# Performance work log

Hardware: AMD Instinct MI355X
Metric: run time of the kernel (lower is better)

Reference implementation:

```python
import jax, jax.numpy as jnp
import numpy as np

B, T, D = 2048, 240, 90  # batch, seq_len (hard-coded 240 in module), hidden
NCLS = 40


def setup_inputs() -> dict:
    key = jax.random.key(0)
    ks = jax.random.split(key, 7)
    s = 1.0 / np.sqrt(D)          # torch LSTMCell init bound
    so = 1.0 / np.sqrt(T * D)     # torch Linear init bound
    x = jax.random.normal(ks[0], (B, T, D), dtype=jnp.float32)
    W_ih = jax.random.uniform(ks[1], (4 * D, D), minval=-s, maxval=s, dtype=jnp.float32)
    W_hh = jax.random.uniform(ks[2], (4 * D, D), minval=-s, maxval=s, dtype=jnp.float32)
    b_ih = jax.random.uniform(ks[3], (4 * D,), minval=-s, maxval=s, dtype=jnp.float32)
    b_hh = jax.random.uniform(ks[4], (4 * D,), minval=-s, maxval=s, dtype=jnp.float32)
    W_out = jax.random.uniform(ks[5], (NCLS, T * D), minval=-so, maxval=so, dtype=jnp.float32)
    b_out = jax.random.uniform(ks[6], (NCLS,), minval=-so, maxval=so, dtype=jnp.float32)
    return {"x": x, "W_ih": W_ih, "W_hh": W_hh, "b_ih": b_ih, "b_hh": b_hh,
            "W_out": W_out, "b_out": b_out}


def reference(x, W_ih, W_hh, b_ih, b_hh, W_out, b_out):
    # The torch loop calls LSTMCell(x[:, i]) with DEFAULT zero (h0, c0) every
    # step -> no recurrence. W_hh @ h0 == 0 and f * c0 == 0, so:
    #   gates = x_t @ W_ih^T + b_ih + b_hh ; gate order i, f, g, o
    gates = jnp.einsum('btd,gd->btg', x, W_ih) + b_ih + b_hh  # [B, T, 4D]
    i_g, _f_g, g_g, o_g = jnp.split(gates, 4, axis=-1)
    c = jax.nn.sigmoid(i_g) * jnp.tanh(g_g)                   # i * g (f*c0 = 0)
    h = jax.nn.sigmoid(o_g) * jnp.tanh(c)                     # [B, T, D]
    out = h.reshape(-1, T * D) @ W_out.T + b_out              # [B, 40]
    out = out.reshape(-1, 4, 10)
    return jax.nn.softmax(out, axis=2)
```

## Files before the change

kernel.cpp:

```cpp
#include <hip/hip_runtime.h>
#include <hip/hip_bf16.h>

#define BB   2048
#define TT   240
#define DD   90
#define HD   96
#define MM   (BB*TT)
#define KDIM (TT*DD)
#define KD2  (TT*HD)
#define NCLS 40
#define NPAD 48
#define KS2  45
#define KST  16

typedef __bf16 bf16x8 __attribute__((ext_vector_type(8)));
typedef float  f32x4  __attribute__((ext_vector_type(4)));

#define LOG2E  1.44269504f
#define LOG2E2 2.88539008f

__device__ __forceinline__ bf16x8 cvt8(float4 a, float4 b){
    bf16x8 r;
    r[0]=(__bf16)a.x; r[1]=(__bf16)a.y; r[2]=(__bf16)a.z; r[3]=(__bf16)a.w;
    r[4]=(__bf16)b.x; r[5]=(__bf16)b.y; r[6]=(__bf16)b.z; r[7]=(__bf16)b.w;
    return r;
}

__device__ __forceinline__ unsigned pack_bf16(float a, float b){
    unsigned u0 = (unsigned)__builtin_bit_cast(unsigned short, (__bf16)a);
    unsigned u1 = (unsigned)__builtin_bit_cast(unsigned short, (__bf16)b);
    return u0 | (u1 << 16);
}

__device__ __forceinline__ float sig_tanh(float a, float b){
    float ea = exp2f(-LOG2E*a);
    float Eb = exp2f(LOG2E2*b);
    return (Eb - 1.f) * __builtin_amdgcn_rcpf((1.f + ea)*(Eb + 1.f));
}

__global__ void pack1(const float* __restrict__ Wih,
                      const float* __restrict__ bih,
                      const float* __restrict__ bhh,
                      __bf16* __restrict__ wtb)
{
    int id = blockIdx.x*256 + threadIdx.x;
    if (id >= 288*13) return;
    int c  = id / 13;
    int k8 = id - c*13;
    int g  = c / 96, dd = c - g*96;
    int row = (g==0 ? dd : (g==1 ? 180+dd : 270+dd));
    float bv = 0.f, bhi = 0.f, blo = 0.f;
    if (dd < 90){
        bv  = bih[row] + bhh[row];
        bhi = (float)(__bf16)bv;
        blo = bv - bhi;
    }
    bf16x8 v;
    #pragma unroll
    for (int e = 0; e < 8; ++e){
        int k = k8*8 + e;
        float f = 0.f;
        if (dd < 90){
            if (k < 90)       f = Wih[row*90 + k];
            else if (k == 90) f = bhi;
            else if (k == 91) f = blo;
        }
        v[e] = (__bf16)f;
    }
    *(bf16x8*)(wtb + c*104 + k8*8) = v;
}

__global__ void pack2(const float* __restrict__ W2,
                      __bf16* __restrict__ w2hi,
                      __bf16* __restrict__ w2lo)
{
    int id = blockIdx.x*256 + threadIdx.x;
    if (id >= NPAD*(KD2/8)) return;
    int n  = id / (KD2/8);
    int k8 = id - n*(KD2/8);
    int t  = k8 / 12;
    int d0 = (k8 - t*12) * 8;
    bf16x8 vh, vl;
    #pragma unroll
    for (int e = 0; e < 8; ++e){
        int d = d0 + e;
        float f = (n < NCLS && d < 90) ? W2[(size_t)n*KDIM + t*90 + d] : 0.f;
        __bf16 hb = (__bf16)f;
        vh[e] = hb;
        vl[e] = (__bf16)(f - (float)hb);
    }
    *(bf16x8*)(w2hi + (size_t)n*KD2 + k8*8) = vh;
    *(bf16x8*)(w2lo + (size_t)n*KD2 + k8*8) = vl;
}

__global__ __launch_bounds__(512, 2)
void k1_gates(const float* __restrict__ x,
              const __bf16* __restrict__ wtb,
              __bf16* __restrict__ h)
{
    __shared__ __align__(16) __bf16 wt[288*104];

    const int tid  = threadIdx.x;
    const int lane = tid & 63;
    const int wv   = tid >> 6;
    const int rg   = wv >> 1;
    const int nh   = wv & 1;
    const int l15  = lane & 15;
    const int kg   = lane >> 4;

    {
        const float4* src = (const float4*)wtb;
        float4* dst = (float4*)wt;
        #pragma unroll
        for (int i = 0; i < 8; ++i){
            int idx = tid + i*512;
            if (idx < 3744) dst[idx] = src[idx];
        }
    }
    __syncthreads();

    const int tbase = blockIdx.x * 15;

    float4 xr[6];
    float2 xe;
    {
        const float* p = x + ((size_t)tbase*64 + rg*16 + l15)*90;
        #pragma unroll
        for (int ks = 0; ks < 2; ++ks){
            xr[ks*2+0] = *(const float4*)(p + ks*32 + kg*8);
            xr[ks*2+1] = *(const float4*)(p + ks*32 + kg*8 + 4);
        }
        if (kg < 3){
            xr[4] = *(const float4*)(p + 64 + kg*8);
            xr[5] = *(const float4*)(p + 64 + kg*8 + 4);
        } else {
            xe = *(const float2*)(p + 88);
        }
    }

    for (int t = 0; t < 15; ++t){
        bf16x8 af[3];
        af[0] = cvt8(xr[0], xr[1]);
        af[1] = cvt8(xr[2], xr[3]);
        if (kg < 3){
            af[2] = cvt8(xr[4], xr[5]);
        } else {
            bf16x8 z;
            #pragma unroll
            for (int e = 0; e < 8; ++e) z[e] = (__bf16)0.f;
            z[0] = (__bf16)xe.x; z[1] = (__bf16)xe.y;
            z[2] = (__bf16)1.0f; z[3] = (__bf16)1.0f;
            af[2] = z;
        }

        if (t < 14){
            const float* p = x + ((size_t)(tbase+t+1)*64 + rg*16 + l15)*90;
            #pragma unroll
            for (int ks = 0; ks < 2; ++ks){
                xr[ks*2+0] = *(const float4*)(p + ks*32 + kg*8);
                xr[ks*2+1] = *(const float4*)(p + ks*32 + kg*8 + 4);
            }
            if (kg < 3){
                xr[4] = *(const float4*)(p + 64 + kg*8);
                xr[5] = *(const float4*)(p + 64 + kg*8 + 4);
            } else {
                xe = *(const float2*)(p + 88);
            }
        }

        f32x4 acc[3][3];
        #pragma unroll
        for (int g = 0; g < 3; ++g)
            #pragma unroll
            for (int j = 0; j < 3; ++j) acc[g][j] = f32x4{0.f,0.f,0.f,0.f};

        const __bf16* wbase = wt + (nh*48 + l15)*104 + 8*kg;
        #pragma unroll
        for (int g = 0; g < 3; ++g){
            #pragma unroll
            for (int j = 0; j < 3; ++j){
                const __bf16* wrow = wbase + (g*96 + j*16)*104;
                #pragma unroll
                for (int ks = 0; ks < 3; ++ks){
                    bf16x8 wv8 = *(const bf16x8*)(wrow + ks*32);
                    acc[g][j] = __builtin_amdgcn_mfma_f32_16x16x32_bf16(wv8, af[ks], acc[g][j], 0,0,0);
                }
            }
        }

        const size_t mrow = (size_t)(tbase+t)*64 + rg*16 + l15;
        __bf16* hp = h + mrow*HD;
        #pragma unroll
        for (int j = 0; j < 3; ++j){
            int dd0 = nh*48 + j*16 + kg*4;
            float hv[4];
            #pragma unroll
            for (int r = 0; r < 4; ++r){
                float cc = sig_tanh(acc[0][j][r], acc[1][j][r]);
                hv[r]    = sig_tanh(acc[2][j][r], cc);
            }
            uint2 pk;
            pk.x = pack_bf16(hv[0], hv[1]);
            pk.y = pack_bf16(hv[2], hv[3]);
            *(uint2*)(hp + dd0) = pk;
        }
    }
}

__global__ __launch_bounds__(256)
void k2_out(const __bf16* __restrict__ h,
            const __bf16* __restrict__ w2hi,
            const __bf16* __restrict__ w2lo,
            float* __restrict__ part2)
{
    const int tid  = threadIdx.x;
    const int lane = tid & 63;
    const int wv   = tid >> 6;
    const int l15  = lane & 15;
    const int kg   = lane >> 4;
    const int m0   = (blockIdx.x*4 + wv) * 32;
    const int chunk= blockIdx.y;
    const size_t kbase = (size_t)chunk*(KST*32) + 8*kg;

    const __bf16* ha = h    + (size_t)(m0 + l15)*KD2 + kbase;
    const __bf16* hb = ha   + (size_t)16*KD2;
    const __bf16* h0 = w2hi + (size_t)l15*KD2 + kbase;
    const __bf16* h1 = h0   + (size_t)16*KD2;
    const __bf16* h2 = h0   + (size_t)32*KD2;
    const __bf16* l0 = w2lo + (size_t)l15*KD2 + kbase;
    const __bf16* l1 = l0   + (size_t)16*KD2;
    const __bf16* l2 = l0   + (size_t)32*KD2;

    f32x4 acc00 = {0.f,0.f,0.f,0.f}, acc01 = acc00, acc02 = acc00;
    f32x4 acc10 = acc00, acc11 = acc00, acc12 = acc00;

    #pragma unroll
    for (int s = 0; s < KST; ++s){
        bf16x8 a0  = *(const bf16x8*)(ha + s*32);
        bf16x8 a1  = *(const bf16x8*)(hb + s*32);
        bf16x8 bh0 = *(const bf16x8*)(h0 + s*32);
        bf16x8 bh1 = *(const bf16x8*)(h1 + s*32);
        bf16x8 bh2 = *(const bf16x8*)(h2 + s*32);
        bf16x8 bl0 = *(const bf16x8*)(l0 + s*32);
        bf16x8 bl1 = *(const bf16x8*)(l1 + s*32);
        bf16x8 bl2 = *(const bf16x8*)(l2 + s*32);
        acc00 = __builtin_amdgcn_mfma_f32_16x16x32_bf16(a0, bh0, acc00, 0,0,0);
        acc01 = __builtin_amdgcn_mfma_f32_16x16x32_bf16(a0, bh1, acc01, 0,0,0);
        acc02 = __builtin_amdgcn_mfma_f32_16x16x32_bf16(a0, bh2, acc02, 0,0,0);
        acc10 = __builtin_amdgcn_mfma_f32_16x16x32_bf16(a1, bh0, acc10, 0,0,0);
        acc11 = __builtin_amdgcn_mfma_f32_16x16x32_bf16(a1, bh1, acc11, 0,0,0);
        acc12 = __builtin_amdgcn_mfma_f32_16x16x32_bf16(a1, bh2, acc12, 0,0,0);
        acc00 = __builtin_amdgcn_mfma_f32_16x16x32_bf16(a0, bl0, acc00, 0,0,0);
        acc01 = __builtin_amdgcn_mfma_f32_16x16x32_bf16(a0, bl1, acc01, 0,0,0);
        acc02 = __builtin_amdgcn_mfma_f32_16x16x32_bf16(a0, bl2, acc02, 0,0,0);
        acc10 = __builtin_amdgcn_mfma_f32_16x16x32_bf16(a1, bl0, acc10, 0,0,0);
        acc11 = __builtin_amdgcn_mfma_f32_16x16x32_bf16(a1, bl1, acc11, 0,0,0);
        acc12 = __builtin_amdgcn_mfma_f32_16x16x32_bf16(a1, bl2, acc12, 0,0,0);
    }

    float* pp = part2 + (size_t)chunk*(BB*NPAD);
    const int rbase = kg*4;
    #pragma unroll
    for (int r = 0; r < 4; ++r){
        size_t row0 = (size_t)(m0 + rbase + r)*NPAD;
        size_t row1 = (size_t)(m0 + 16 + rbase + r)*NPAD;
        pp[row0 +      l15] = acc00[r];
        pp[row0 + 16 + l15] = acc01[r];
        pp[row0 + 32 + l15] = acc02[r];
        pp[row1 +      l15] = acc10[r];
        pp[row1 + 16 + l15] = acc11[r];
        pp[row1 + 32 + l15] = acc12[r];
    }
}

__global__ __launch_bounds__(384)
void k3(const float* __restrict__ part2,
        const float* __restrict__ bout,
        float* __restrict__ out)
{
    __shared__ float sm[8*NPAD];
    const int tid  = threadIdx.x;
    const int base = blockIdx.x * 8 * NPAD;

    {
        int g = base + tid;
        float s = 0.f;
        for (int c = 0; c < KS2; ++c) s += part2[(size_t)c*(BB*NPAD) + g];
        int n = tid % NPAD;
        sm[tid] = s + (n < NCLS ? bout[n] : 0.f);
    }
    __syncthreads();

    if (tid < 32){
        int lb  = tid >> 2;
        int grp = tid & 3;
        const float* lg = sm + lb*NPAD + grp*10;
        float v[10]; float mx = -1e30f;
        #pragma unroll
        for (int q = 0; q < 10; ++q){ v[q] = lg[q]; mx = fmaxf(mx, v[q]); }
        float e[10]; float s = 0.f;
        #pragma unroll
        for (int q = 0; q < 10; ++q){ e[q] = __expf(v[q]-mx); s += e[q]; }
        float inv = 1.0f/s;
        size_t b = (size_t)blockIdx.x*8 + lb;
        #pragma unroll
        for (int q = 0; q < 10; ++q) out[b*NCLS + grp*10 + q] = e[q]*inv;
    }
}

extern "C" void kernel_launch(void* const* d_in, const int* in_sizes, int n_in,
                              void* d_out, int out_size, void* d_ws, size_t ws_size,
                              hipStream_t stream)
{
    const float* x    = (const float*)d_in[0];
    const float* Wih  = (const float*)d_in[1];
    const float* bih  = (const float*)d_in[3];
    const float* bhh  = (const float*)d_in[4];
    const float* W2   = (const float*)d_in[5];
    const float* bout = (const float*)d_in[6];
    float* out = (float*)d_out;

    char* ws = (char*)d_ws;
    size_t off = 0;
    auto alloc = [&](size_t bytes){ void* p = ws + off; off = (off + bytes + 255) & ~(size_t)255; return p; };
    __bf16* h     = (__bf16*)alloc((size_t)MM*HD*2);
    float*  part2 = (float*) alloc((size_t)KS2*BB*NPAD*4);
    __bf16* wtb   = (__bf16*)alloc(288*104*2);
    __bf16* w2hi  = (__bf16*)alloc((size_t)NPAD*KD2*2);
    __bf16* w2lo  = (__bf16*)alloc((size_t)NPAD*KD2*2);

    pack1<<<15, 256, 0, stream>>>(Wih, bih, bhh, wtb);
    pack2<<<(NPAD*(KD2/8) + 255)/256, 256, 0, stream>>>(W2, w2hi, w2lo);
    k1_gates<<<512, 512, 0, stream>>>(x, wtb, h);
    k2_out<<<dim3(16, KS2), 256, 0, stream>>>(h, w2hi, w2lo, part2);
    k3<<<BB/8, 384, 0, stream>>>(part2, bout, out);
}
```

Measured before the change: 146.4 us.

## Split gate kernel across hidden-column panels with register-resident weights

The gate kernel grid now gains a dimension of three column panels. Each wave keeps its 16-column slice of the input weights in registers instead of staging the whole weight matrix in shared memory, so it issues only 9 MFMAs per step instead of 27. The hidden state is written in a panel-major layout (three panels of 32 columns). The output GEMM kernel and the W_out packing are re-indexed to match, so each K-chunk reads a contiguous panel. In exchange, every x tile is now loaded three times, once per panel, which triples the kernel's input reads.

```diff
diff --git a/kernel.cpp b/kernel.cpp
--- a/kernel.cpp
+++ b/kernel.cpp
@@ -4,10 +4,10 @@
 #define BB   2048
 #define TT   240
 #define DD   90
-#define HD   96
 #define MM   (BB*TT)
 #define KDIM (TT*DD)
-#define KD2  (TT*HD)
+#define KD2  23040
+#define PSTRIDE ((size_t)MM*32)
 #define NCLS 40
 #define NPAD 48
 #define KS2  45
@@ -76,21 +76,24 @@
 {
     int id = blockIdx.x*256 + threadIdx.x;
     if (id >= NPAD*(KD2/8)) return;
-    int n  = id / (KD2/8);
-    int k8 = id - n*(KD2/8);
-    int t  = k8 / 12;
-    int d0 = (k8 - t*12) * 8;
+    int n   = id / (KD2/8);
+    int k8  = id - n*(KD2/8);
+    int kk  = k8*8;
+    int p   = kk / 7680;
+    int rem = kk - p*7680;
+    int t   = rem / 32;
+    int ddl = rem - t*32;
     bf16x8 vh, vl;
     #pragma unroll
     for (int e = 0; e < 8; ++e){
-        int d = d0 + e;
+        int d = p*32 + ddl + e;
         float f = (n < NCLS && d < 90) ? W2[(size_t)n*KDIM + t*90 + d] : 0.f;
         __bf16 hb = (__bf16)f;
         vh[e] = hb;
         vl[e] = (__bf16)(f - (float)hb);
     }
-    *(bf16x8*)(w2hi + (size_t)n*KD2 + k8*8) = vh;
-    *(bf16x8*)(w2lo + (size_t)n*KD2 + k8*8) = vl;
+    *(bf16x8*)(w2hi + (size_t)n*KD2 + kk) = vh;
+    *(bf16x8*)(w2lo + (size_t)n*KD2 + kk) = vl;
 }
 
 __global__ __launch_bounds__(512, 2)
@@ -98,28 +101,26 @@
               const __bf16* __restrict__ wtb,
               __bf16* __restrict__ h)
 {
-    __shared__ __align__(16) __bf16 wt[288*104];
-
     const int tid  = threadIdx.x;
     const int lane = tid & 63;
     const int wv   = tid >> 6;
     const int rg   = wv >> 1;
-    const int nh   = wv & 1;
+    const int csl  = wv & 1;
+    const int cs   = blockIdx.y*2 + csl;
     const int l15  = lane & 15;
     const int kg   = lane >> 4;
 
-    {
-        const float4* src = (const float4*)wtb;
-        float4* dst = (float4*)wt;
-        #pragma unroll
-        for (int i = 0; i < 8; ++i){
-            int idx = tid + i*512;
-            if (idx < 3744) dst[idx] = src[idx];
-        }
-    }
-    __syncthreads();
+    bf16x8 wf[3][3];
+    #pragma unroll
+    for (int g = 0; g < 3; ++g){
+        const __bf16* wp = wtb + (g*96 + cs*16 + l15)*104 + kg*8;
+        #pragma unroll
+        for (int ks = 0; ks < 3; ++ks)
+            wf[g][ks] = *(const bf16x8*)(wp + ks*32);
+    }
 
     const int tbase = blockIdx.x * 15;
+    __bf16* hpanel = h + (size_t)blockIdx.y*PSTRIDE;
 
     float4 xr[6];
     float2 xe;
@@ -168,42 +169,25 @@
             }
         }
 
-        f32x4 acc[3][3];
-        #pragma unroll
-        for (int g = 0; g < 3; ++g)
-            #pragma unroll
-            for (int j = 0; j < 3; ++j) acc[g][j] = f32x4{0.f,0.f,0.f,0.f};
-
-        const __bf16* wbase = wt + (nh*48 + l15)*104 + 8*kg;
-        #pragma unroll
-        for (int g = 0; g < 3; ++g){
-            #pragma unroll
-            for (int j = 0; j < 3; ++j){
-                const __bf16* wrow = wbase + (g*96 + j*16)*104;
-                #pragma unroll
-                for (int ks = 0; ks < 3; ++ks){
-                    bf16x8 wv8 = *(const bf16x8*)(wrow + ks*32);
-                    acc[g][j] = __builtin_amdgcn_mfma_f32_16x16x32_bf16(wv8, af[ks], acc[g][j], 0,0,0);
-                }
-            }
-        }
-
+        f32x4 acc0 = {0.f,0.f,0.f,0.f}, acc1 = acc0, acc2 = acc0;
+        #pragma unroll
+        for (int ks = 0; ks < 3; ++ks){
+            acc0 = __builtin_amdgcn_mfma_f32_16x16x32_bf16(wf[0][ks], af[ks], acc0, 0,0,0);
+            acc1 = __builtin_amdgcn_mfma_f32_16x16x32_bf16(wf[1][ks], af[ks], acc1, 0,0,0);
+            acc2 = __builtin_amdgcn_mfma_f32_16x16x32_bf16(wf[2][ks], af[ks], acc2, 0,0,0);
+        }
+
+        float hv[4];
+        #pragma unroll
+        for (int r = 0; r < 4; ++r){
+            float cc = sig_tanh(acc0[r], acc1[r]);
+            hv[r]    = sig_tanh(acc2[r], cc);
+        }
         const size_t mrow = (size_t)(tbase+t)*64 + rg*16 + l15;
-        __bf16* hp = h + mrow*HD;
-        #pragma unroll
-        for (int j = 0; j < 3; ++j){
-            int dd0 = nh*48 + j*16 + kg*4;
-            float hv[4];
-            #pragma unroll
-            for (int r = 0; r < 4; ++r){
-                float cc = sig_tanh(acc[0][j][r], acc[1][j][r]);
-                hv[r]    = sig_tanh(acc[2][j][r], cc);
-            }
-            uint2 pk;
-            pk.x = pack_bf16(hv[0], hv[1]);
-            pk.y = pack_bf16(hv[2], hv[3]);
-            *(uint2*)(hp + dd0) = pk;
-        }
+        uint2 pk;
+        pk.x = pack_bf16(hv[0], hv[1]);
+        pk.y = pack_bf16(hv[2], hv[3]);
+        *(uint2*)(hpanel + mrow*32 + csl*16 + kg*4) = pk;
     }
 }
 
@@ -220,10 +204,13 @@
     const int kg   = lane >> 4;
     const int m0   = (blockIdx.x*4 + wv) * 32;
     const int chunk= blockIdx.y;
+    const int p    = chunk / 15;
+    const int t0   = (chunk - p*15) * 16;
+
+    const __bf16* ha = h + (size_t)p*PSTRIDE
+                         + ((size_t)(m0 + l15)*240 + t0)*32 + 8*kg;
+    const __bf16* hb = ha + (size_t)16*240*32;
     const size_t kbase = (size_t)chunk*(KST*32) + 8*kg;
-
-    const __bf16* ha = h    + (size_t)(m0 + l15)*KD2 + kbase;
-    const __bf16* hb = ha   + (size_t)16*KD2;
     const __bf16* h0 = w2hi + (size_t)l15*KD2 + kbase;
     const __bf16* h1 = h0   + (size_t)16*KD2;
     const __bf16* h2 = h0   + (size_t)32*KD2;
@@ -323,7 +310,7 @@
     char* ws = (char*)d_ws;
     size_t off = 0;
     auto alloc = [&](size_t bytes){ void* p = ws + off; off = (off + bytes + 255) & ~(size_t)255; return p; };
-    __bf16* h     = (__bf16*)alloc((size_t)MM*HD*2);
+    __bf16* h     = (__bf16*)alloc((size_t)3*PSTRIDE*2);
     float*  part2 = (float*) alloc((size_t)KS2*BB*NPAD*4);
     __bf16* wtb   = (__bf16*)alloc(288*104*2);
     __bf16* w2hi  = (__bf16*)alloc((size_t)NPAD*KD2*2);
@@ -331,7 +318,7 @@
 
     pack1<<<15, 256, 0, stream>>>(Wih, bih, bhh, wtb);
     pack2<<<(NPAD*(KD2/8) + 255)/256, 256, 0, stream>>>(W2, w2hi, w2lo);
-    k1_gates<<<512, 512, 0, stream>>>(x, wtb, h);
+    k1_gates<<<dim3(512, 3), 512, 0, stream>>>(x, wtb, h);
     k2_out<<<dim3(16, KS2), 256, 0, stream>>>(h, w2hi, w2lo, part2);
     k3<<<BB/8, 384, 0, stream>>>(part2, bout, out);
 }
```

Result: slower. 176.5 us (+20.5%).
